# Kernel optimization log

Hardware: AMD Instinct MI355X
Metric: run time of the kernel (lower is better)

## Reference

```python
import jax, jax.numpy as jnp
import numpy as np

B = 4194304  # batch rows
DX = 10      # input feature dim (hardcoded in module)
DH = 4       # hidden dim (hardcoded in module)


def setup_inputs() -> dict:
    key = jax.random.key(0)
    ks = jax.random.split(key, 14)
    s_in = 1.0 / np.sqrt(DX)
    s_h = 1.0 / np.sqrt(DH)
    return {
        "x": jax.random.normal(ks[0], (B, DX), jnp.float32),
        "hidden": jax.random.normal(ks[1], (B, DH), jnp.float32),
        # torch.nn.Linear weights: W has shape [out, in], y = x @ W.T + b
        "Wzh": jax.random.uniform(ks[2], (DH, DH), jnp.float32, -s_h, s_h),
        "bzh": jax.random.uniform(ks[3], (DH,), jnp.float32, -s_h, s_h),
        "Wzx": jax.random.uniform(ks[4], (DH, DX), jnp.float32, -s_in, s_in),
        "bzx": jax.random.uniform(ks[5], (DH,), jnp.float32, -s_in, s_in),
        "Wrh": jax.random.uniform(ks[6], (DH, DH), jnp.float32, -s_h, s_h),
        "brh": jax.random.uniform(ks[7], (DH,), jnp.float32, -s_h, s_h),
        "Wrx": jax.random.uniform(ks[8], (DH, DX), jnp.float32, -s_in, s_in),
        "brx": jax.random.uniform(ks[9], (DH,), jnp.float32, -s_in, s_in),
        "Wnx": jax.random.uniform(ks[10], (DH, DX), jnp.float32, -s_in, s_in),
        "bnx": jax.random.uniform(ks[11], (DH,), jnp.float32, -s_in, s_in),
        "Wnh": jax.random.uniform(ks[12], (DH, DH), jnp.float32, -s_h, s_h),
        "bnh": jax.random.uniform(ks[13], (DH,), jnp.float32, -s_h, s_h),
    }


def reference(x, hidden, Wzh, bzh, Wzx, bzx, Wrh, brh, Wrx, brx, Wnx, bnx, Wnh, bnh):
    # z = sigmoid(hidden @ Wzh.T + bzh + x @ Wzx.T + bzx)
    z = jax.nn.sigmoid(hidden @ Wzh.T + bzh + x @ Wzx.T + bzx)
    r = jax.nn.sigmoid(hidden @ Wrh.T + brh + x @ Wrx.T + brx)
    n = jnp.tanh(r * (hidden @ Wnh.T + bnh) + x @ Wnx.T + bnx)
    return (1.0 - z) * n + z * hidden
```

## Files before the change

kernel.cpp:

```cpp
#include <hip/hip_runtime.h>
#include <math.h>


constexpr int DXc = 10;
constexpr int DHc = 4;

__global__ __launch_bounds__(256, 4)
void gru_fused(const float* __restrict__ x,
               const float* __restrict__ hidden,
               const float* __restrict__ Wzh, const float* __restrict__ bzh,
               const float* __restrict__ Wzx, const float* __restrict__ bzx,
               const float* __restrict__ Wrh, const float* __restrict__ brh,
               const float* __restrict__ Wrx, const float* __restrict__ brx,
               const float* __restrict__ Wnx, const float* __restrict__ bnx,
               const float* __restrict__ Wnh, const float* __restrict__ bnh,
               float* __restrict__ out, int total )
{
    const int tid = blockIdx.x * blockDim.x + threadIdx.x;
    const int nth = gridDim.x * blockDim.x;
    const int j   = tid & 3;

    float wzh[DHc], wrh[DHc], wnh[DHc];
    float wzx[DXc], wrx[DXc], wnx[DXc];
#pragma unroll
    for (int k = 0; k < DHc; ++k) {
        wzh[k] = Wzh[j * DHc + k];
        wrh[k] = Wrh[j * DHc + k];
        wnh[k] = Wnh[j * DHc + k];
    }
#pragma unroll
    for (int k = 0; k < DXc; ++k) {
        wzx[k] = Wzx[j * DXc + k];
        wrx[k] = Wrx[j * DXc + k];
        wnx[k] = Wnx[j * DXc + k];
    }
    const float bz    = bzh[j] + bzx[j];
    const float br    = brh[j] + brx[j];
    const float bnh_j = bnh[j];
    const float bnx_j = bnx[j];

    for (int p = tid; p < total; p += nth) {
        const int row = p >> 2;

        const float2* xr = reinterpret_cast<const float2*>(x + row * DXc);
        float xv[DXc];
#pragma unroll
        for (int q = 0; q < DXc / 2; ++q) {
            const float2 t = xr[q];
            xv[2 * q]     = t.x;
            xv[2 * q + 1] = t.y;
        }
        const float4 hv = *reinterpret_cast<const float4*>(hidden + row * DHc);
        const float hvv[DHc] = {hv.x, hv.y, hv.z, hv.w};

        float az = bz, ar = br, ah = bnh_j, ax = bnx_j;
#pragma unroll
        for (int k = 0; k < DHc; ++k) {
            az = fmaf(hvv[k], wzh[k], az);
            ar = fmaf(hvv[k], wrh[k], ar);
            ah = fmaf(hvv[k], wnh[k], ah);
        }
#pragma unroll
        for (int k = 0; k < DXc; ++k) {
            az = fmaf(xv[k], wzx[k], az);
            ar = fmaf(xv[k], wrx[k], ar);
            ax = fmaf(xv[k], wnx[k], ax);
        }

        const float z = 1.0f / (1.0f + expf(-az));
        const float r = 1.0f / (1.0f + expf(-ar));
        const float n = tanhf(fmaf(r, ah, ax));

        const float hj = (j < 2) ? (j == 0 ? hv.x : hv.y)
                                 : (j == 2 ? hv.z : hv.w);

        out[p] = fmaf(z, hj - n, n);
    }
}

extern "C" void kernel_launch(void* const* d_in, const int* in_sizes, int n_in,
                              void* d_out, int out_size, void* d_ws, size_t ws_size,
                              hipStream_t stream) {
    const float* x   = (const float*)d_in[0];
    const float* h   = (const float*)d_in[1];
    const float* Wzh = (const float*)d_in[2];
    const float* bzh = (const float*)d_in[3];
    const float* Wzx = (const float*)d_in[4];
    const float* bzx = (const float*)d_in[5];
    const float* Wrh = (const float*)d_in[6];
    const float* brh = (const float*)d_in[7];
    const float* Wrx = (const float*)d_in[8];
    const float* brx = (const float*)d_in[9];
    const float* Wnx = (const float*)d_in[10];
    const float* bnx = (const float*)d_in[11];
    const float* Wnh = (const float*)d_in[12];
    const float* bnh = (const float*)d_in[13];
    float* out = (float*)d_out;

    const int total = out_size;
    const int block = 256;
    const int grid  = 2048;

    gru_fused<<<grid, block, 0, stream>>>(x, h, Wzh, bzh, Wzx, bzx,
                                          Wrh, brh, Wrx, brx,
                                          Wnx, bnx, Wnh, bnh, out, total);
}
```

Baseline: 335.6 us.

## Stage x tiles in LDS, make weights wave-uniform, use fast exp/rcp activations

Each block now loads a 512-row tile of x into shared memory with coalesced float4 loads. Each wavefront handles one output column, so its weights are wave-uniform and kept in scalar registers via readfirstlane. Results are transposed through LDS so the output stores coalesce. Sigmoid and tanh use pre-scaled exp2 and rcp intrinsics in place of expf/tanhf. The launch changes from a grid-stride loop to one block per tile, which assumes the row count divides evenly by 512. The fast intrinsics give slightly less precise results.

```diff
diff --git a/kernel.cpp b/kernel.cpp
--- a/kernel.cpp
+++ b/kernel.cpp
@@ -1,9 +1,14 @@
 #include <hip/hip_runtime.h>
-#include <math.h>
 
 
 constexpr int DXc = 10;
 constexpr int DHc = 4;
+constexpr int TR  = 512;
+constexpr int XF4 = TR * DXc / 4;
+
+__device__ __forceinline__ float sgpr_f(float v) {
+    return __uint_as_float(__builtin_amdgcn_readfirstlane(__float_as_uint(v)));
+}
 
 __global__ __launch_bounds__(256, 4)
 void gru_fused(const float* __restrict__ x,
@@ -14,67 +19,97 @@
                const float* __restrict__ Wrx, const float* __restrict__ brx,
                const float* __restrict__ Wnx, const float* __restrict__ bnx,
                const float* __restrict__ Wnh, const float* __restrict__ bnh,
-               float* __restrict__ out, int total )
+               float* __restrict__ out)
 {
-    const int tid = blockIdx.x * blockDim.x + threadIdx.x;
-    const int nth = gridDim.x * blockDim.x;
-    const int j   = tid & 3;
+    __shared__ float xs[TR * DXc];
+
+    const int t    = threadIdx.x;
+    const int lane = t & 63;
+    const int j    = __builtin_amdgcn_readfirstlane(t >> 6);
+    const int tile = blockIdx.x * TR;
+
+    {
+        const float4* xg = reinterpret_cast<const float4*>(x) + blockIdx.x * XF4;
+        float4* xl = reinterpret_cast<float4*>(xs);
+#pragma unroll
+        for (int q = 0; q < 5; ++q)
+            xl[q * 256 + t] = xg[q * 256 + t];
+    }
+
+    const float kL2E = 1.44269504088896f;
+    const float sZ = -kL2E;
+    const float sN = 2.0f * kL2E;
 
     float wzh[DHc], wrh[DHc], wnh[DHc];
     float wzx[DXc], wrx[DXc], wnx[DXc];
 #pragma unroll
     for (int k = 0; k < DHc; ++k) {
-        wzh[k] = Wzh[j * DHc + k];
-        wrh[k] = Wrh[j * DHc + k];
-        wnh[k] = Wnh[j * DHc + k];
+        wzh[k] = sgpr_f(Wzh[j * DHc + k] * sZ);
+        wrh[k] = sgpr_f(Wrh[j * DHc + k] * sZ);
+        wnh[k] = sgpr_f(Wnh[j * DHc + k] * sN);
     }
 #pragma unroll
     for (int k = 0; k < DXc; ++k) {
-        wzx[k] = Wzx[j * DXc + k];
-        wrx[k] = Wrx[j * DXc + k];
-        wnx[k] = Wnx[j * DXc + k];
+        wzx[k] = sgpr_f(Wzx[j * DXc + k] * sZ);
+        wrx[k] = sgpr_f(Wrx[j * DXc + k] * sZ);
+        wnx[k] = sgpr_f(Wnx[j * DXc + k] * sN);
     }
-    const float bz    = bzh[j] + bzx[j];
-    const float br    = brh[j] + brx[j];
-    const float bnh_j = bnh[j];
-    const float bnx_j = bnx[j];
+    const float bz    = sgpr_f((bzh[j] + bzx[j]) * sZ);
+    const float br    = sgpr_f((brh[j] + brx[j]) * sZ);
+    const float bnh_j = sgpr_f(bnh[j] * sN);
+    const float bnx_j = sgpr_f(bnx[j] * sN);
 
-    for (int p = tid; p < total; p += nth) {
-        const int row = p >> 2;
+    __syncthreads();
 
-        const float2* xr = reinterpret_cast<const float2*>(x + row * DXc);
-        float xv[DXc];
+    float o[8];
 #pragma unroll
-        for (int q = 0; q < DXc / 2; ++q) {
-            const float2 t = xr[q];
-            xv[2 * q]     = t.x;
-            xv[2 * q + 1] = t.y;
-        }
-        const float4 hv = *reinterpret_cast<const float4*>(hidden + row * DHc);
+    for (int k = 0; k < 8; ++k) {
+        const int rl = lane + (k << 6);
+
+        const float2* xr = reinterpret_cast<const float2*>(xs + rl * DXc);
+        const float2 a0 = xr[0], a1 = xr[1], a2 = xr[2], a3 = xr[3], a4 = xr[4];
+        const float xv[DXc] = {a0.x, a0.y, a1.x, a1.y, a2.x,
+                               a2.y, a3.x, a3.y, a4.x, a4.y};
+
+        const float4 hv = *reinterpret_cast<const float4*>(hidden + (tile + rl) * DHc);
         const float hvv[DHc] = {hv.x, hv.y, hv.z, hv.w};
 
         float az = bz, ar = br, ah = bnh_j, ax = bnx_j;
 #pragma unroll
-        for (int k = 0; k < DHc; ++k) {
-            az = fmaf(hvv[k], wzh[k], az);
-            ar = fmaf(hvv[k], wrh[k], ar);
-            ah = fmaf(hvv[k], wnh[k], ah);
+        for (int c = 0; c < DHc; ++c) {
+            az = fmaf(hvv[c], wzh[c], az);
+            ar = fmaf(hvv[c], wrh[c], ar);
+            ah = fmaf(hvv[c], wnh[c], ah);
         }
 #pragma unroll
-        for (int k = 0; k < DXc; ++k) {
-            az = fmaf(xv[k], wzx[k], az);
-            ar = fmaf(xv[k], wrx[k], ar);
-            ax = fmaf(xv[k], wnx[k], ax);
+        for (int c = 0; c < DXc; ++c) {
+            az = fmaf(xv[c], wzx[c], az);
+            ar = fmaf(xv[c], wrx[c], ar);
+            ax = fmaf(xv[c], wnx[c], ax);
         }
 
-        const float z = 1.0f / (1.0f + expf(-az));
-        const float r = 1.0f / (1.0f + expf(-ar));
-        const float n = tanhf(fmaf(r, ah, ax));
+        const float z  = __builtin_amdgcn_rcpf(1.0f + __builtin_amdgcn_exp2f(az));
+        const float r  = __builtin_amdgcn_rcpf(1.0f + __builtin_amdgcn_exp2f(ar));
+        const float tt = fmaf(r, ah, ax);
+        const float n  = fmaf(-2.0f,
+                              __builtin_amdgcn_rcpf(1.0f + __builtin_amdgcn_exp2f(tt)),
+                              1.0f);
 
-        const float hj = (j < 2) ? (j == 0 ? hv.x : hv.y)
-                                 : (j == 2 ? hv.z : hv.w);
+        const float hj = (j == 0) ? hv.x : (j == 1) ? hv.y : (j == 2) ? hv.z : hv.w;
+        o[k] = fmaf(z, hj - n, n);
+    }
 
-        out[p] = fmaf(z, hj - n, n);
+    __syncthreads();
+#pragma unroll
+    for (int k = 0; k < 8; ++k)
+        xs[(lane + (k << 6)) * 5 + j] = o[k];
+    __syncthreads();
+
+    float* op = out + tile * DHc;
+#pragma unroll
+    for (int k = 0; k < 8; ++k) {
+        const int m = (k << 8) + t;
+        op[m] = xs[(m >> 2) * 5 + (t & 3)];
     }
 }
 
@@ -97,11 +132,9 @@
     const float* bnh = (const float*)d_in[13];
     float* out = (float*)d_out;
 
-    const int total = out_size;
-    const int block = 256;
-    const int grid  = 2048;
-
-    gru_fused<<<grid, block, 0, stream>>>(x, h, Wzh, bzh, Wzx, bzx,
-                                          Wrh, brh, Wrx, brx,
-                                          Wnx, bnx, Wnh, bnh, out, total);
+    const int nrows = out_size / DHc;
+    const int grid  = nrows / TR;
+    gru_fused<<<grid, 256, 0, stream>>>(x, h, Wzh, bzh, Wzx, bzx,
+                                        Wrh, brh, Wrx, brx,
+                                        Wnx, bnx, Wnh, bnh, out);
 }
```

Measured after the change: 311.4 us. 1.08x faster.
